# Performance work log

Measured on AMD Instinct MI355X. Metric: run time of the kernel, lower is better.

Reference implementation:

```python
import jax, jax.numpy as jnp
import numpy as np

INPUT_DIM = 32
HID_DIM = 64
TTCN_DIM = HID_DIM - 1  # 63
N, LX = 128, 512


def setup_inputs() -> dict:
    key = jax.random.key(0)
    ks = jax.random.split(key, 10)
    X_int = jax.random.normal(ks[0], (N, LX, INPUT_DIM), dtype=jnp.float32)
    mask_X = jax.random.randint(ks[1], (N, LX, 1), 0, 2).astype(jnp.float32)
    s1 = 1.0 / np.sqrt(INPUT_DIM)
    s2 = 1.0 / np.sqrt(TTCN_DIM)
    W1 = jax.random.uniform(ks[2], (INPUT_DIM, TTCN_DIM), jnp.float32, -s1, s1)
    b1 = jax.random.uniform(ks[3], (TTCN_DIM,), jnp.float32, -s1, s1)
    W2 = jax.random.uniform(ks[4], (TTCN_DIM, TTCN_DIM), jnp.float32, -s2, s2)
    b2 = jax.random.uniform(ks[5], (TTCN_DIM,), jnp.float32, -s2, s2)
    W3 = jax.random.uniform(ks[6], (TTCN_DIM, INPUT_DIM * TTCN_DIM), jnp.float32, -s2, s2)
    b3 = jax.random.uniform(ks[7], (INPUT_DIM * TTCN_DIM,), jnp.float32, -s2, s2)
    T_bias = jax.random.normal(ks[8], (1, TTCN_DIM), dtype=jnp.float32)
    return {"X_int": X_int, "mask_X": mask_X, "W1": W1, "b1": b1,
            "W2": W2, "b2": b2, "W3": W3, "b3": b3, "T_bias": T_bias}


def reference(X_int, mask_X, W1, b1, W2, b2, W3, b3, T_bias):
    n, lx, d = X_int.shape
    k = TTCN_DIM
    # 3-layer MLP filter generator: (N, Lx, D*K)
    h = jax.nn.relu(X_int @ W1 + b1)
    h = jax.nn.relu(h @ W2 + b2)
    filt = h @ W3 + b3
    # masked softmax over the time axis Lx
    filt = filt * mask_X + (1.0 - mask_X) * (-1e8)
    filt = jax.nn.softmax(filt, axis=1)  # softmax over Lx
    filt = filt.reshape(n, lx, k, d)     # (N, Lx, K, D)
    # attention-weighted pooling: sum over Lx and D
    out = jnp.einsum('nld,nlkd->nk', X_int, filt)
    return jax.nn.relu(out + T_bias)
```

## Files before the change

kernel.cpp:

```cpp
#include <hip/hip_runtime.h>
#include <hip/hip_bf16.h>


#define N_   128
#define LX_  512
#define D_   32
#define K_   63
#define C_   2016
#define LOG2E 1.44269504088896f

typedef __bf16 bf16x8 __attribute__((ext_vector_type(8)));
typedef float floatx4 __attribute__((ext_vector_type(4)));
typedef float floatx2 __attribute__((ext_vector_type(2)));

static __device__ __forceinline__ floatx4 mfma16(bf16x8 a, bf16x8 b, floatx4 c) {
  return __builtin_amdgcn_mfma_f32_16x16x32_bf16(a, b, c, 0, 0, 0);
}

#define HC_OFF   0u
#define XT_OFF   (8u * 1024u * 1024u)
#define W3FR_OFF (16u * 1024u * 1024u)
#define W1FR_OFF (W3FR_OFF + 258048u)
#define W2FR_OFF (W1FR_OFF + 4096u)
#define B1_OFF   (W2FR_OFF + 8192u)
#define POS_OFF  (B1_OFF + 256u)
#define CNT_OFF  (POS_OFF + 262144u)

__global__ __launch_bounds__(256) void kern_prep(
    const float* __restrict__ Mk,
    const float* __restrict__ W1, const float* __restrict__ b1,
    const float* __restrict__ W2, const float* __restrict__ b2,
    const float* __restrict__ W3, const float* __restrict__ b3,
    __bf16* __restrict__ W3fr, __bf16* __restrict__ W1fr,
    __bf16* __restrict__ W2fr, float* __restrict__ b1pad,
    int* __restrict__ pos, int* __restrict__ cnt,
    __bf16* __restrict__ Hc, float* __restrict__ Xt) {
  const int n = blockIdx.x, tid = threadIdx.x;
  __shared__ int s_cnt;

  if (tid < 64) {
    const int lane = tid;
    int running = 0;
    for (int c = 0; c < 8; ++c) {
      const int l = c * 64 + lane;
      const float mkv = Mk[n * LX_ + l];
      const unsigned long long b = __ballot(mkv > 0.5f);
      const int mypos = running + __popcll(b & ((1ull << lane) - 1ull));
      pos[n * LX_ + l] = (mkv > 0.5f) ? mypos : -1;
      running += __popcll(b);
    }
    if (lane == 0) { cnt[n] = running; s_cnt = running; }
  }
  __syncthreads();

  const int c0 = s_cnt, c1 = (c0 + 63) & ~63;
  const float4 z = {0.f, 0.f, 0.f, 0.f};
  for (int idx = tid; idx < (c1 - c0) * 40; idx += 256) {
    const int row = c0 + idx / 40, q = idx % 40;
    if (q < 8) {
      *(float4*)(Hc + ((size_t)(n * 512 + row)) * 64 + q * 8) = z;
    } else {
      const int d = q - 8;
      Xt[((size_t)(n * 32 + (row >> 4)) * 32 + d) * 16 + (row & 15)] = 0.f;
    }
  }

  for (int g = n * 256 + tid; g < 129024 + 2048 + 4096 + 64; g += N_ * 256) {
    if (g < 129024) {
      const int j = g & 7, quad = (g >> 3) & 3, l16 = (g >> 5) & 15, h = (g >> 9) & 1;
      const int rest = g >> 10, i = rest % 6, tile = rest / 6;
      const int c = tile * 96 + i * 16 + l16;
      const int t = h * 32 + quad * 8 + j;
      W3fr[g] = (__bf16)(((t < K_) ? W3[(size_t)t * C_ + c] : b3[c]) * LOG2E);
    } else if (g < 129024 + 2048) {
      const int g2 = g - 129024;
      const int j = g2 & 7, quad = (g2 >> 3) & 3, l16 = (g2 >> 5) & 15, i = g2 >> 9;
      const int ch = i * 16 + l16, t = quad * 8 + j;
      W1fr[g2] = (__bf16)((ch < K_) ? W1[t * K_ + ch] : 0.f);
    } else if (g < 129024 + 2048 + 4096) {
      const int g2 = g - 129024 - 2048;
      const int j = g2 & 7, quad = (g2 >> 3) & 3, l16 = (g2 >> 5) & 15, h = (g2 >> 9) & 1;
      const int i = g2 >> 10;
      const int ch = i * 16 + l16, t = h * 32 + quad * 8 + j;
      float v;
      if (t < K_) v = (ch < K_) ? W2[t * K_ + ch] : 0.f;
      else        v = (ch < K_) ? b2[ch] : 1.f;
      W2fr[g2] = (__bf16)v;
    } else {
      const int g2 = g - 129024 - 2048 - 4096;
      b1pad[g2] = (g2 < K_) ? b1[g2] : 0.f;
    }
  }
}

__global__ __launch_bounds__(256) void kern_mlp(
    const float* __restrict__ X, const __bf16* __restrict__ W1fr,
    const __bf16* __restrict__ W2fr, const float* __restrict__ b1pad,
    const int* __restrict__ pos, __bf16* __restrict__ Hc,
    float* __restrict__ Xt) {
  __shared__ float h1s[4][16][68];
  const int tid = threadIdx.x;
  const int w = tid >> 6, lane = tid & 63, quad = lane >> 4, l16 = lane & 15;

  bf16x8 b1f[4], b2f[4][2];
  float b1v[4];
#pragma unroll
  for (int i = 0; i < 4; ++i) {
    b1f[i]    = *(const bf16x8*)(W1fr + ((i * 16 + l16) * 4 + quad) * 8);
    b2f[i][0] = *(const bf16x8*)(W2fr + (((i * 2 + 0) * 16 + l16) * 4 + quad) * 8);
    b2f[i][1] = *(const bf16x8*)(W2fr + (((i * 2 + 1) * 16 + l16) * 4 + quad) * 8);
    b1v[i] = b1pad[i * 16 + l16];
  }

  const int tok0 = blockIdx.x * 64 + w * 16;
  const int n = tok0 >> 9;
  const float* xp = X + (size_t)(tok0 + l16) * D_ + quad * 8;
  const float4 xa = *(const float4*)xp;
  const float4 xb = *(const float4*)(xp + 4);
  bf16x8 a1;
  a1[0]=(__bf16)xa.x; a1[1]=(__bf16)xa.y; a1[2]=(__bf16)xa.z; a1[3]=(__bf16)xa.w;
  a1[4]=(__bf16)xb.x; a1[5]=(__bf16)xb.y; a1[6]=(__bf16)xb.z; a1[7]=(__bf16)xb.w;

  const int px = pos[tok0 + l16];
  int pr[4];
#pragma unroll
  for (int r = 0; r < 4; ++r) pr[r] = pos[tok0 + quad * 4 + r];

  if (px >= 0) {
    float* xtp = Xt + ((size_t)(n * 32 + (px >> 4)) * 32 + quad * 8) * 16 + (px & 15);
    const float vals[8] = {xa.x, xa.y, xa.z, xa.w, xb.x, xb.y, xb.z, xb.w};
#pragma unroll
    for (int j = 0; j < 8; ++j) xtp[j * 16] = vals[j];
  }

#pragma unroll
  for (int i = 0; i < 4; ++i) {
    floatx4 acc = {0.f, 0.f, 0.f, 0.f};
    acc = mfma16(a1, b1f[i], acc);
#pragma unroll
    for (int r = 0; r < 4; ++r) {
      float v = fmaxf(acc[r] + b1v[i], 0.f);
      if (i == 3 && l16 == 15) v = 1.f;
      h1s[w][quad * 4 + r][i * 16 + l16] = v;
    }
  }

  const float* hrow = &h1s[w][l16][0];
  const float4 p0 = *(const float4*)(hrow + quad * 8);
  const float4 p1 = *(const float4*)(hrow + quad * 8 + 4);
  const float4 p2 = *(const float4*)(hrow + 32 + quad * 8);
  const float4 p3 = *(const float4*)(hrow + 32 + quad * 8 + 4);
  bf16x8 a20, a21;
  a20[0]=(__bf16)p0.x; a20[1]=(__bf16)p0.y; a20[2]=(__bf16)p0.z; a20[3]=(__bf16)p0.w;
  a20[4]=(__bf16)p1.x; a20[5]=(__bf16)p1.y; a20[6]=(__bf16)p1.z; a20[7]=(__bf16)p1.w;
  a21[0]=(__bf16)p2.x; a21[1]=(__bf16)p2.y; a21[2]=(__bf16)p2.z; a21[3]=(__bf16)p2.w;
  a21[4]=(__bf16)p3.x; a21[5]=(__bf16)p3.y; a21[6]=(__bf16)p3.z; a21[7]=(__bf16)p3.w;

#pragma unroll
  for (int i = 0; i < 4; ++i) {
    floatx4 acc = {0.f, 0.f, 0.f, 0.f};
    acc = mfma16(a20, b2f[i][0], acc);
    acc = mfma16(a21, b2f[i][1], acc);
#pragma unroll
    for (int r = 0; r < 4; ++r) {
      if (pr[r] >= 0)
        Hc[((size_t)(n * 512 + pr[r])) * 64 + i * 16 + l16] =
            (__bf16)fmaxf(acc[r], 0.f);
    }
  }
}

__global__ __launch_bounds__(256) void kern_att(
    const __bf16* __restrict__ Hc, const float* __restrict__ Xt,
    const __bf16* __restrict__ W3fr, const int* __restrict__ cnt,
    const float* __restrict__ Tb, float* __restrict__ out) {
  __shared__ float redS[4][96], redO[4][96];
  __shared__ float rbuf[96];

  const int bid = blockIdx.x;
  const int idx = bid >> 3;
  const int n = (bid & 7) * 16 + idx / 21;
  const int bt = idx % 21;
  const int tid = threadIdx.x;
  const int w = tid >> 6, lane = tid & 63, quad = lane >> 4, l16 = lane & 15;

  bf16x8 bf[6][2];
#pragma unroll
  for (int i = 0; i < 6; ++i) {
    bf[i][0] = *(const bf16x8*)(W3fr + ((((bt * 6 + i) * 2 + 0) * 16 + l16) * 4 + quad) * 8);
    bf[i][1] = *(const bf16x8*)(W3fr + ((((bt * 6 + i) * 2 + 1) * 16 + l16) * 4 + quad) * 8);
  }

  const int cntn = cnt[n];
  const int nch = (cntn + 15) >> 4;
  const __bf16* Hb = Hc + ((size_t)n << 9) * 64 + (size_t)l16 * 64 + quad * 8;
  const float*  Xb = Xt + ((size_t)n * 32) * 512 + l16 * 16 + quad * 4;

  floatx2 s2[3] = {{0.f, 0.f}, {0.f, 0.f}, {0.f, 0.f}};
  float o[6] = {0, 0, 0, 0, 0, 0};

  int c = w;
  bf16x8 a0 = *(const bf16x8*)(Hb + (size_t)c * 1024);
  bf16x8 a1 = *(const bf16x8*)(Hb + (size_t)c * 1024 + 32);
  float4 xl4 = *(const float4*)(Xb + c * 512);
  float4 xh4 = *(const float4*)(Xb + c * 512 + 256);

#pragma unroll 1
  while (c < nch) {
    const int cn = c + 4;
    bf16x8 na0, na1;
    float4 nxl, nxh;
    if (cn < nch) {
      na0 = *(const bf16x8*)(Hb + (size_t)cn * 1024);
      na1 = *(const bf16x8*)(Hb + (size_t)cn * 1024 + 32);
      nxl = *(const float4*)(Xb + cn * 512);
      nxh = *(const float4*)(Xb + cn * 512 + 256);
    }

#pragma unroll
    for (int t = 0; t < 3; ++t) {
      floatx4 accE = {0.f, 0.f, 0.f, 0.f};
      floatx4 accO = {0.f, 0.f, 0.f, 0.f};
      accE = mfma16(a0, bf[2 * t][0], accE);
      accE = mfma16(a1, bf[2 * t][1], accE);
      accO = mfma16(a0, bf[2 * t + 1][0], accO);
      accO = mfma16(a1, bf[2 * t + 1][1], accO);
#pragma unroll
      for (int r = 0; r < 4; ++r) {
        floatx2 e2;
        e2.x = __builtin_amdgcn_exp2f(accE[r]);
        e2.y = __builtin_amdgcn_exp2f(accO[r]);
        s2[t] += e2;
        o[2 * t]     = fmaf(e2.x, xl4[r], o[2 * t]);
        o[2 * t + 1] = fmaf(e2.y, xh4[r], o[2 * t + 1]);
      }
    }

    c = cn;
    a0 = na0; a1 = na1; xl4 = nxl; xh4 = nxh;
  }

#pragma unroll
  for (int t = 0; t < 3; ++t) {
    s2[t].x += __shfl_xor(s2[t].x, 16); s2[t].x += __shfl_xor(s2[t].x, 32);
    s2[t].y += __shfl_xor(s2[t].y, 16); s2[t].y += __shfl_xor(s2[t].y, 32);
  }
#pragma unroll
  for (int i = 0; i < 6; ++i) {
    o[i] += __shfl_xor(o[i], 16);
    o[i] += __shfl_xor(o[i], 32);
  }
  if (quad == 0) {
#pragma unroll
    for (int t = 0; t < 3; ++t) {
      redS[w][(2 * t) * 16 + l16]     = s2[t].x;
      redS[w][(2 * t + 1) * 16 + l16] = s2[t].y;
    }
#pragma unroll
    for (int i = 0; i < 6; ++i) redO[w][i * 16 + l16] = o[i];
  }
  __syncthreads();
  if (tid < 96) {
    const float pad = (float)(nch * 16 - cntn);
    const float S = redS[0][tid] + redS[1][tid] + redS[2][tid] + redS[3][tid] - pad;
    const float O = redO[0][tid] + redO[1][tid] + redO[2][tid] + redO[3][tid];
    rbuf[tid] = O / S;
  }
  __syncthreads();
  if (tid < 3) {
    float acc = 0.f;
#pragma unroll
    for (int dd = 0; dd < 32; ++dd) acc += rbuf[tid * 32 + dd];
    const int k = bt * 3 + tid;
    out[n * K_ + k] = fmaxf(acc + Tb[k], 0.f);
  }
}

extern "C" void kernel_launch(void* const* d_in, const int* in_sizes, int n_in,
                              void* d_out, int out_size, void* d_ws, size_t ws_size,
                              hipStream_t stream) {
  const float* X  = (const float*)d_in[0];
  const float* Mk = (const float*)d_in[1];
  const float* W1 = (const float*)d_in[2];
  const float* b1 = (const float*)d_in[3];
  const float* W2 = (const float*)d_in[4];
  const float* b2 = (const float*)d_in[5];
  const float* W3 = (const float*)d_in[6];
  const float* b3 = (const float*)d_in[7];
  const float* Tb = (const float*)d_in[8];
  float* out = (float*)d_out;

  char* ws = (char*)d_ws;
  __bf16* Hc    = (__bf16*)(ws + HC_OFF);
  float*  Xt    = (float*)(ws + XT_OFF);
  __bf16* W3fr  = (__bf16*)(ws + W3FR_OFF);
  __bf16* W1fr  = (__bf16*)(ws + W1FR_OFF);
  __bf16* W2fr  = (__bf16*)(ws + W2FR_OFF);
  float*  b1pad = (float*)(ws + B1_OFF);
  int*    pos   = (int*)(ws + POS_OFF);
  int*    cnt   = (int*)(ws + CNT_OFF);

  kern_prep<<<N_, 256, 0, stream>>>(Mk, W1, b1, W2, b2, W3, b3,
                                    W3fr, W1fr, W2fr, b1pad, pos, cnt, Hc, Xt);
  kern_mlp<<<N_ * LX_ / 64, 256, 0, stream>>>(X, W1fr, W2fr, b1pad, pos, Hc, Xt);
  kern_att<<<N_ * 21, 256, 0, stream>>>(Hc, Xt, W3fr, cnt, Tb, out);
}
```

Baseline: 112.9 us.

## Fuse prep into MLP kernel and process two batches per attention block

Removes the separate prep kernel. Each MLP block now recomputes the mask prefix scan for its batch and builds its W1/W2 bf16 fragments straight from the fp32 weights. The same blocks also zero the tail padding and write their share of the W3 fragment table. The attention kernel now handles two batch rows per block, so each W3 fragment load is reused across both, and it uses a new XCD-aware block mapping and a launch_bounds occupancy hint. In exchange there is redundant per-block scan and weight-conversion work, and the software prefetch of the next chunk is dropped.

```diff
diff --git a/kernel.cpp b/kernel.cpp
--- a/kernel.cpp
+++ b/kernel.cpp
@@ -20,100 +20,69 @@
 #define HC_OFF   0u
 #define XT_OFF   (8u * 1024u * 1024u)
 #define W3FR_OFF (16u * 1024u * 1024u)
-#define W1FR_OFF (W3FR_OFF + 258048u)
-#define W2FR_OFF (W1FR_OFF + 4096u)
-#define B1_OFF   (W2FR_OFF + 8192u)
-#define POS_OFF  (B1_OFF + 256u)
-#define CNT_OFF  (POS_OFF + 262144u)
-
-__global__ __launch_bounds__(256) void kern_prep(
-    const float* __restrict__ Mk,
+#define CNT_OFF  (W3FR_OFF + 262144u)
+
+__global__ __launch_bounds__(256) void kern_mlp(
+    const float* __restrict__ X, const float* __restrict__ Mk,
     const float* __restrict__ W1, const float* __restrict__ b1,
     const float* __restrict__ W2, const float* __restrict__ b2,
     const float* __restrict__ W3, const float* __restrict__ b3,
-    __bf16* __restrict__ W3fr, __bf16* __restrict__ W1fr,
-    __bf16* __restrict__ W2fr, float* __restrict__ b1pad,
-    int* __restrict__ pos, int* __restrict__ cnt,
-    __bf16* __restrict__ Hc, float* __restrict__ Xt) {
-  const int n = blockIdx.x, tid = threadIdx.x;
+    __bf16* __restrict__ Hc, float* __restrict__ Xt,
+    __bf16* __restrict__ W3fr, int* __restrict__ cnt) {
+  __shared__ int pos_s[64];
   __shared__ int s_cnt;
-
-  if (tid < 64) {
-    const int lane = tid;
-    int running = 0;
-    for (int c = 0; c < 8; ++c) {
-      const int l = c * 64 + lane;
-      const float mkv = Mk[n * LX_ + l];
-      const unsigned long long b = __ballot(mkv > 0.5f);
-      const int mypos = running + __popcll(b & ((1ull << lane) - 1ull));
-      pos[n * LX_ + l] = (mkv > 0.5f) ? mypos : -1;
-      running += __popcll(b);
-    }
-    if (lane == 0) { cnt[n] = running; s_cnt = running; }
-  }
-  __syncthreads();
-
-  const int c0 = s_cnt, c1 = (c0 + 63) & ~63;
-  const float4 z = {0.f, 0.f, 0.f, 0.f};
-  for (int idx = tid; idx < (c1 - c0) * 40; idx += 256) {
-    const int row = c0 + idx / 40, q = idx % 40;
-    if (q < 8) {
-      *(float4*)(Hc + ((size_t)(n * 512 + row)) * 64 + q * 8) = z;
-    } else {
-      const int d = q - 8;
-      Xt[((size_t)(n * 32 + (row >> 4)) * 32 + d) * 16 + (row & 15)] = 0.f;
-    }
-  }
-
-  for (int g = n * 256 + tid; g < 129024 + 2048 + 4096 + 64; g += N_ * 256) {
-    if (g < 129024) {
-      const int j = g & 7, quad = (g >> 3) & 3, l16 = (g >> 5) & 15, h = (g >> 9) & 1;
-      const int rest = g >> 10, i = rest % 6, tile = rest / 6;
-      const int c = tile * 96 + i * 16 + l16;
-      const int t = h * 32 + quad * 8 + j;
-      W3fr[g] = (__bf16)(((t < K_) ? W3[(size_t)t * C_ + c] : b3[c]) * LOG2E);
-    } else if (g < 129024 + 2048) {
-      const int g2 = g - 129024;
-      const int j = g2 & 7, quad = (g2 >> 3) & 3, l16 = (g2 >> 5) & 15, i = g2 >> 9;
-      const int ch = i * 16 + l16, t = quad * 8 + j;
-      W1fr[g2] = (__bf16)((ch < K_) ? W1[t * K_ + ch] : 0.f);
-    } else if (g < 129024 + 2048 + 4096) {
-      const int g2 = g - 129024 - 2048;
-      const int j = g2 & 7, quad = (g2 >> 3) & 3, l16 = (g2 >> 5) & 15, h = (g2 >> 9) & 1;
-      const int i = g2 >> 10;
-      const int ch = i * 16 + l16, t = h * 32 + quad * 8 + j;
-      float v;
-      if (t < K_) v = (ch < K_) ? W2[t * K_ + ch] : 0.f;
-      else        v = (ch < K_) ? b2[ch] : 1.f;
-      W2fr[g2] = (__bf16)v;
-    } else {
-      const int g2 = g - 129024 - 2048 - 4096;
-      b1pad[g2] = (g2 < K_) ? b1[g2] : 0.f;
-    }
-  }
-}
-
-__global__ __launch_bounds__(256) void kern_mlp(
-    const float* __restrict__ X, const __bf16* __restrict__ W1fr,
-    const __bf16* __restrict__ W2fr, const float* __restrict__ b1pad,
-    const int* __restrict__ pos, __bf16* __restrict__ Hc,
-    float* __restrict__ Xt) {
   __shared__ float h1s[4][16][68];
+
   const int tid = threadIdx.x;
   const int w = tid >> 6, lane = tid & 63, quad = lane >> 4, l16 = lane & 15;
+  const int bid = blockIdx.x;
+  const int tok0b = bid * 64;
+  const int n = bid >> 3, blk8 = bid & 7;
+
+  if (tid < 64) {
+    int running = 0;
+#pragma unroll
+    for (int c = 0; c < 8; ++c) {
+      const float mkv = Mk[n * LX_ + c * 64 + tid];
+      const unsigned long long b = __ballot(mkv > 0.5f);
+      const int mypos = running + __popcll(b & ((1ull << tid) - 1ull));
+      if (c == blk8) pos_s[tid] = (mkv > 0.5f) ? mypos : -1;
+      running += __popcll(b);
+    }
+    if (tid == 0) {
+      s_cnt = running;
+      if (blk8 == 0) cnt[n] = running;
+    }
+  }
 
   bf16x8 b1f[4], b2f[4][2];
   float b1v[4];
 #pragma unroll
   for (int i = 0; i < 4; ++i) {
-    b1f[i]    = *(const bf16x8*)(W1fr + ((i * 16 + l16) * 4 + quad) * 8);
-    b2f[i][0] = *(const bf16x8*)(W2fr + (((i * 2 + 0) * 16 + l16) * 4 + quad) * 8);
-    b2f[i][1] = *(const bf16x8*)(W2fr + (((i * 2 + 1) * 16 + l16) * 4 + quad) * 8);
-    b1v[i] = b1pad[i * 16 + l16];
-  }
-
-  const int tok0 = blockIdx.x * 64 + w * 16;
-  const int n = tok0 >> 9;
+    const int ch = i * 16 + l16;
+    const int chc = (ch < K_) ? ch : 62;
+#pragma unroll
+    for (int j = 0; j < 8; ++j) {
+      const int t = quad * 8 + j;
+      b1f[i][j] = (__bf16)((ch < K_) ? W1[t * K_ + chc] : 0.f);
+    }
+    b1v[i] = (ch < K_) ? b1[chc] : 0.f;
+    const float b2c = (ch < K_) ? b2[chc] : 0.f;
+#pragma unroll
+    for (int h = 0; h < 2; ++h) {
+#pragma unroll
+      for (int j = 0; j < 8; ++j) {
+        const int t = h * 32 + quad * 8 + j;
+        const float w2v = W2[((t < K_) ? t : 62) * K_ + chc];
+        float v;
+        if (ch < K_) v = (t < K_) ? w2v : b2c;
+        else         v = (t < K_) ? 0.f : 1.f;
+        b2f[i][h][j] = (__bf16)v;
+      }
+    }
+  }
+
+  const int tok0 = tok0b + w * 16;
   const float* xp = X + (size_t)(tok0 + l16) * D_ + quad * 8;
   const float4 xa = *(const float4*)xp;
   const float4 xb = *(const float4*)(xp + 4);
@@ -121,10 +90,10 @@
   a1[0]=(__bf16)xa.x; a1[1]=(__bf16)xa.y; a1[2]=(__bf16)xa.z; a1[3]=(__bf16)xa.w;
   a1[4]=(__bf16)xb.x; a1[5]=(__bf16)xb.y; a1[6]=(__bf16)xb.z; a1[7]=(__bf16)xb.w;
 
-  const int px = pos[tok0 + l16];
-  int pr[4];
-#pragma unroll
-  for (int r = 0; r < 4; ++r) pr[r] = pos[tok0 + quad * 4 + r];
+  __syncthreads();
+
+  const int px = pos_s[w * 16 + l16];
+  const int4 pr4 = *(const int4*)&pos_s[w * 16 + quad * 4];
 
   if (px >= 0) {
     float* xtp = Xt + ((size_t)(n * 32 + (px >> 4)) * 32 + quad * 8) * 16 + (px & 15);
@@ -156,6 +125,7 @@
   a21[0]=(__bf16)p2.x; a21[1]=(__bf16)p2.y; a21[2]=(__bf16)p2.z; a21[3]=(__bf16)p2.w;
   a21[4]=(__bf16)p3.x; a21[5]=(__bf16)p3.y; a21[6]=(__bf16)p3.z; a21[7]=(__bf16)p3.w;
 
+  const int pr[4] = {pr4.x, pr4.y, pr4.z, pr4.w};
 #pragma unroll
   for (int i = 0; i < 4; ++i) {
     floatx4 acc = {0.f, 0.f, 0.f, 0.f};
@@ -168,19 +138,38 @@
             (__bf16)fmaxf(acc[r], 0.f);
     }
   }
+
+  if (blk8 == 7) {
+    const int c0 = s_cnt, c1 = (c0 + 15) & ~15;
+    const float4 z = {0.f, 0.f, 0.f, 0.f};
+    for (int idx2 = tid; idx2 < (c1 - c0) * 40; idx2 += 256) {
+      const int row = c0 + idx2 / 40, q = idx2 % 40;
+      if (q < 8) *(float4*)(Hc + ((size_t)(n * 512 + row)) * 64 + q * 8) = z;
+      else Xt[((size_t)(n * 32 + (row >> 4)) * 32 + (q - 8)) * 16 + (row & 15)] = 0.f;
+    }
+  }
+
+  const int g = bid * 256 + tid;
+  if (g < 129024) {
+    const int j2 = g & 7, q2 = (g >> 3) & 3, l2 = (g >> 5) & 15, h2 = (g >> 9) & 1;
+    const int rest = g >> 10, i2 = rest % 6, tile = rest / 6;
+    const int c = tile * 96 + i2 * 16 + l2;
+    const int t = h2 * 32 + q2 * 8 + j2;
+    W3fr[g] = (__bf16)(((t < K_) ? W3[(size_t)t * C_ + c] : b3[c]) * LOG2E);
+  }
 }
 
-__global__ __launch_bounds__(256) void kern_att(
+__global__ __launch_bounds__(256, 3) void kern_att(
     const __bf16* __restrict__ Hc, const float* __restrict__ Xt,
     const __bf16* __restrict__ W3fr, const int* __restrict__ cnt,
     const float* __restrict__ Tb, float* __restrict__ out) {
-  __shared__ float redS[4][96], redO[4][96];
-  __shared__ float rbuf[96];
+  __shared__ float redS[4][192], redO[4][192];
+  __shared__ float rbuf[192];
 
   const int bid = blockIdx.x;
-  const int idx = bid >> 3;
-  const int n = (bid & 7) * 16 + idx / 21;
-  const int bt = idx % 21;
+  const int xcd = bid & 7, g = bid >> 3;
+  const int npl = g & 7, bt = g >> 3;
+  const int n0 = (xcd * 8 + npl) * 2;
   const int tid = threadIdx.x;
   const int w = tid >> 6, lane = tid & 63, quad = lane >> 4, l16 = lane & 15;
 
@@ -191,88 +180,101 @@
     bf[i][1] = *(const bf16x8*)(W3fr + ((((bt * 6 + i) * 2 + 1) * 16 + l16) * 4 + quad) * 8);
   }
 
-  const int cntn = cnt[n];
-  const int nch = (cntn + 15) >> 4;
-  const __bf16* Hb = Hc + ((size_t)n << 9) * 64 + (size_t)l16 * 64 + quad * 8;
-  const float*  Xb = Xt + ((size_t)n * 32) * 512 + l16 * 16 + quad * 4;
-
-  floatx2 s2[3] = {{0.f, 0.f}, {0.f, 0.f}, {0.f, 0.f}};
-  float o[6] = {0, 0, 0, 0, 0, 0};
-
-  int c = w;
-  bf16x8 a0 = *(const bf16x8*)(Hb + (size_t)c * 1024);
-  bf16x8 a1 = *(const bf16x8*)(Hb + (size_t)c * 1024 + 32);
-  float4 xl4 = *(const float4*)(Xb + c * 512);
-  float4 xh4 = *(const float4*)(Xb + c * 512 + 256);
+  const int cnt0 = cnt[n0], cnt1 = cnt[n0 + 1];
+  const int nch0 = (cnt0 + 15) >> 4, nch1 = (cnt1 + 15) >> 4;
+  const int nchm = (nch0 > nch1) ? nch0 : nch1;
+  const __bf16* Hb0 = Hc + ((size_t)n0 << 9) * 64 + l16 * 64 + quad * 8;
+  const __bf16* Hb1 = Hb0 + (size_t)512 * 64;
+  const float*  Xb0 = Xt + (size_t)n0 * 16384 + l16 * 16 + quad * 4;
+  const float*  Xb1 = Xb0 + 16384;
+
+  floatx2 s2[2][3], o2[2][3];
+#pragma unroll
+  for (int ni = 0; ni < 2; ++ni)
+#pragma unroll
+    for (int t = 0; t < 3; ++t) { s2[ni][t] = {0.f, 0.f}; o2[ni][t] = {0.f, 0.f}; }
 
 #pragma unroll 1
-  while (c < nch) {
-    const int cn = c + 4;
-    bf16x8 na0, na1;
-    float4 nxl, nxh;
-    if (cn < nch) {
-      na0 = *(const bf16x8*)(Hb + (size_t)cn * 1024);
-      na1 = *(const bf16x8*)(Hb + (size_t)cn * 1024 + 32);
-      nxl = *(const float4*)(Xb + cn * 512);
-      nxh = *(const float4*)(Xb + cn * 512 + 256);
-    }
-
+  for (int c = w; c < nchm; c += 4) {
+    const bool d0 = c < nch0, d1 = c < nch1;
+    bf16x8 A0[2], A1[2];
+    float4 XL[2], XH[2];
+    if (d0) {
+      A0[0] = *(const bf16x8*)(Hb0 + (size_t)c * 1024);
+      A1[0] = *(const bf16x8*)(Hb0 + (size_t)c * 1024 + 32);
+      XL[0] = *(const float4*)(Xb0 + c * 512);
+      XH[0] = *(const float4*)(Xb0 + c * 512 + 256);
+    }
+    if (d1) {
+      A0[1] = *(const bf16x8*)(Hb1 + (size_t)c * 1024);
+      A1[1] = *(const bf16x8*)(Hb1 + (size_t)c * 1024 + 32);
+      XL[1] = *(const float4*)(Xb1 + c * 512);
+      XH[1] = *(const float4*)(Xb1 + c * 512 + 256);
+    }
+#pragma unroll
+    for (int ni = 0; ni < 2; ++ni) {
+      if (ni ? d1 : d0) {
+#pragma unroll
+        for (int t = 0; t < 3; ++t) {
+          floatx4 accE = {0.f, 0.f, 0.f, 0.f};
+          floatx4 accO = {0.f, 0.f, 0.f, 0.f};
+          accE = mfma16(A0[ni], bf[2 * t][0], accE);
+          accE = mfma16(A1[ni], bf[2 * t][1], accE);
+          accO = mfma16(A0[ni], bf[2 * t + 1][0], accO);
+          accO = mfma16(A1[ni], bf[2 * t + 1][1], accO);
+#pragma unroll
+          for (int r = 0; r < 4; ++r) {
+            floatx2 e2, x2;
+            e2.x = __builtin_amdgcn_exp2f(accE[r]);
+            e2.y = __builtin_amdgcn_exp2f(accO[r]);
+            x2.x = XL[ni][r];
+            x2.y = XH[ni][r];
+            s2[ni][t] += e2;
+            o2[ni][t] += e2 * x2;
+          }
+        }
+      }
+    }
+  }
+
+#pragma unroll
+  for (int ni = 0; ni < 2; ++ni)
 #pragma unroll
     for (int t = 0; t < 3; ++t) {
-      floatx4 accE = {0.f, 0.f, 0.f, 0.f};
-      floatx4 accO = {0.f, 0.f, 0.f, 0.f};
-      accE = mfma16(a0, bf[2 * t][0], accE);
-      accE = mfma16(a1, bf[2 * t][1], accE);
-      accO = mfma16(a0, bf[2 * t + 1][0], accO);
-      accO = mfma16(a1, bf[2 * t + 1][1], accO);
-#pragma unroll
-      for (int r = 0; r < 4; ++r) {
-        floatx2 e2;
-        e2.x = __builtin_amdgcn_exp2f(accE[r]);
-        e2.y = __builtin_amdgcn_exp2f(accO[r]);
-        s2[t] += e2;
-        o[2 * t]     = fmaf(e2.x, xl4[r], o[2 * t]);
-        o[2 * t + 1] = fmaf(e2.y, xh4[r], o[2 * t + 1]);
+      s2[ni][t].x += __shfl_xor(s2[ni][t].x, 16); s2[ni][t].x += __shfl_xor(s2[ni][t].x, 32);
+      s2[ni][t].y += __shfl_xor(s2[ni][t].y, 16); s2[ni][t].y += __shfl_xor(s2[ni][t].y, 32);
+      o2[ni][t].x += __shfl_xor(o2[ni][t].x, 16); o2[ni][t].x += __shfl_xor(o2[ni][t].x, 32);
+      o2[ni][t].y += __shfl_xor(o2[ni][t].y, 16); o2[ni][t].y += __shfl_xor(o2[ni][t].y, 32);
+    }
+  if (quad == 0) {
+#pragma unroll
+    for (int ni = 0; ni < 2; ++ni)
+#pragma unroll
+      for (int t = 0; t < 3; ++t) {
+        redS[w][ni * 96 + (2 * t) * 16 + l16]     = s2[ni][t].x;
+        redS[w][ni * 96 + (2 * t + 1) * 16 + l16] = s2[ni][t].y;
+        redO[w][ni * 96 + (2 * t) * 16 + l16]     = o2[ni][t].x;
+        redO[w][ni * 96 + (2 * t + 1) * 16 + l16] = o2[ni][t].y;
       }
-    }
-
-    c = cn;
-    a0 = na0; a1 = na1; xl4 = nxl; xh4 = nxh;
-  }
-
-#pragma unroll
-  for (int t = 0; t < 3; ++t) {
-    s2[t].x += __shfl_xor(s2[t].x, 16); s2[t].x += __shfl_xor(s2[t].x, 32);
-    s2[t].y += __shfl_xor(s2[t].y, 16); s2[t].y += __shfl_xor(s2[t].y, 32);
-  }
-#pragma unroll
-  for (int i = 0; i < 6; ++i) {
-    o[i] += __shfl_xor(o[i], 16);
-    o[i] += __shfl_xor(o[i], 32);
-  }
-  if (quad == 0) {
-#pragma unroll
-    for (int t = 0; t < 3; ++t) {
-      redS[w][(2 * t) * 16 + l16]     = s2[t].x;
-      redS[w][(2 * t + 1) * 16 + l16] = s2[t].y;
-    }
-#pragma unroll
-    for (int i = 0; i < 6; ++i) redO[w][i * 16 + l16] = o[i];
   }
   __syncthreads();
-  if (tid < 96) {
-    const float pad = (float)(nch * 16 - cntn);
+  if (tid < 192) {
+    const int ni = tid / 96;
+    const int cc = ni ? cnt1 : cnt0;
+    const int nc = ni ? nch1 : nch0;
+    const float pad = (float)(nc * 16 - cc);
     const float S = redS[0][tid] + redS[1][tid] + redS[2][tid] + redS[3][tid] - pad;
     const float O = redO[0][tid] + redO[1][tid] + redO[2][tid] + redO[3][tid];
     rbuf[tid] = O / S;
   }
   __syncthreads();
-  if (tid < 3) {
+  if (tid < 6) {
+    const int ni = tid / 3, kk = tid % 3;
     float acc = 0.f;
 #pragma unroll
-    for (int dd = 0; dd < 32; ++dd) acc += rbuf[tid * 32 + dd];
-    const int k = bt * 3 + tid;
-    out[n * K_ + k] = fmaxf(acc + Tb[k], 0.f);
+    for (int dd = 0; dd < 32; ++dd) acc += rbuf[ni * 96 + kk * 32 + dd];
+    const int k = bt * 3 + kk;
+    out[(n0 + ni) * K_ + k] = fmaxf(acc + Tb[k], 0.f);
   }
 }
 
@@ -291,17 +293,12 @@
   float* out = (float*)d_out;
 
   char* ws = (char*)d_ws;
-  __bf16* Hc    = (__bf16*)(ws + HC_OFF);
-  float*  Xt    = (float*)(ws + XT_OFF);
-  __bf16* W3fr  = (__bf16*)(ws + W3FR_OFF);
-  __bf16* W1fr  = (__bf16*)(ws + W1FR_OFF);
-  __bf16* W2fr  = (__bf16*)(ws + W2FR_OFF);
-  float*  b1pad = (float*)(ws + B1_OFF);
-  int*    pos   = (int*)(ws + POS_OFF);
-  int*    cnt   = (int*)(ws + CNT_OFF);
-
-  kern_prep<<<N_, 256, 0, stream>>>(Mk, W1, b1, W2, b2, W3, b3,
-                                    W3fr, W1fr, W2fr, b1pad, pos, cnt, Hc, Xt);
-  kern_mlp<<<N_ * LX_ / 64, 256, 0, stream>>>(X, W1fr, W2fr, b1pad, pos, Hc, Xt);
-  kern_att<<<N_ * 21, 256, 0, stream>>>(Hc, Xt, W3fr, cnt, Tb, out);
+  __bf16* Hc   = (__bf16*)(ws + HC_OFF);
+  float*  Xt   = (float*)(ws + XT_OFF);
+  __bf16* W3fr = (__bf16*)(ws + W3FR_OFF);
+  int*    cnt  = (int*)(ws + CNT_OFF);
+
+  kern_mlp<<<1024, 256, 0, stream>>>(X, Mk, W1, b1, W2, b2, W3, b3,
+                                     Hc, Xt, W3fr, cnt);
+  kern_att<<<1344, 256, 0, stream>>>(Hc, Xt, W3fr, cnt, Tb, out);
 }
```

Result: slower. 118.4 us (+4.9%).
